# Performance work log

Hardware: AMD Instinct MI355X
Metric: run time of the kernel (lower is better)

## Reference

```python
import jax, jax.numpy as jnp
import numpy as np
import math

B, S, HID = 2, 1024, 2048
H, KV, HD = 32, 8, 64
GROUPS = H // KV
KB_N = 4096
THETA = 10000.0


def _rope_cos_sin(position_ids, head_dim, theta=THETA):
    inv_freq = 1.0 / (theta ** (jnp.arange(0, head_dim, 2, dtype=jnp.float32) / head_dim))
    ang = position_ids.astype(jnp.float32)[..., None] * inv_freq  # [B,S,hd/2]
    cos = jnp.concatenate([jnp.cos(ang), jnp.cos(ang)], -1)[:, None]  # [B,1,S,hd]
    sin = jnp.concatenate([jnp.sin(ang), jnp.sin(ang)], -1)[:, None]
    return cos, sin


def _rotate_half(x):
    h = x.shape[-1] // 2
    return jnp.concatenate([-x[..., h:], x[..., :h]], -1)


def _apply_rope(x, cos, sin):
    return x * cos + _rotate_half(x) * sin


def setup_inputs() -> dict:
    key = jax.random.key(0)
    ks = jax.random.split(key, 10)
    hidden_states = jax.random.normal(ks[0], (B, S, HID), dtype=jnp.float32)
    causal = jnp.where(jnp.tril(jnp.ones((S, S), bool)), 0.0, -1e9).astype(jnp.float32)
    attention_mask = jnp.broadcast_to(causal[None, None], (B, 1, S, S)).copy()
    kb_keys = jax.random.normal(ks[1], (B, KB_N, HD), dtype=jnp.float32)
    kb_values = jax.random.normal(ks[2], (B, KB_N, HD), dtype=jnp.float32)
    position_ids = jnp.broadcast_to(jnp.arange(S, dtype=jnp.int64 if jax.config.read('jax_enable_x64') else jnp.int32)[None], (B, S))
    s = 0.02
    Wq = jax.random.normal(ks[3], (HID, HID), dtype=jnp.float32) * s
    Wq_kb = jax.random.normal(ks[4], (HID, HID), dtype=jnp.float32) * s
    Wk = jax.random.normal(ks[5], (KV * HD, HID), dtype=jnp.float32) * s
    Wv = jax.random.normal(ks[6], (KV * HD, HID), dtype=jnp.float32) * s
    Wo = jax.random.normal(ks[7], (HID, HID), dtype=jnp.float32) * s
    score_shift = jnp.zeros((H, 1), dtype=jnp.float32) - 3.0
    return {"hidden_states": hidden_states, "attention_mask": attention_mask,
            "kb_keys": kb_keys, "kb_values": kb_values, "Wq": Wq, "Wq_kb": Wq_kb,
            "Wk": Wk, "Wv": Wv, "Wo": Wo, "score_shift": score_shift,
            "position_ids": position_ids, "top_k": 128}


def reference(hidden_states, attention_mask, kb_keys, kb_values, Wq, Wq_kb, Wk, Wv, Wo, score_shift, position_ids, top_k):
    bsz, q_len, _ = hidden_states.shape
    scale = 1.0 / math.sqrt(HD)
    q = (hidden_states @ Wq.T).reshape(bsz, q_len, H, HD).transpose(0, 2, 1, 3)
    k = (hidden_states @ Wk.T).reshape(bsz, q_len, KV, HD).transpose(0, 2, 1, 3)
    v = (hidden_states @ Wv.T).reshape(bsz, q_len, KV, HD).transpose(0, 2, 1, 3)
    k = jnp.repeat(k, GROUPS, axis=1)  # repeat_kv
    v = jnp.repeat(v, GROUPS, axis=1)
    cos, sin = _rope_cos_sin(position_ids, HD)
    q = _apply_rope(q, cos, sin)
    k = _apply_rope(k, cos, sin)
    attn = jnp.einsum('bhsd,bhtd->bhst', q, k) * scale
    # KB path (layer_idx=0, kb_layer_frequency=1, sep_query_head, dynamic_sparsify)
    qkb = (hidden_states @ Wq_kb.T).reshape(bsz, q_len, H, HD).transpose(0, 2, 1, 3)
    qkb = _apply_rope(qkb, cos, sin)
    kb_scores = jnp.einsum('bhsd,bnd->bhsn', qkb, kb_keys) * scale  # [B,H,S,N]
    # prune_key_value: top-k over head/seq-summed scores, gather keys/values (no grad)
    top_idx = jax.lax.stop_gradient(jax.lax.top_k(kb_scores.sum((1, 2)), top_k)[1])  # [B,k]
    kb_k_g = jax.lax.stop_gradient(jnp.take_along_axis(kb_keys, top_idx[..., None], axis=1))  # [B,k,hd]
    kb_v_g = jax.lax.stop_gradient(jnp.take_along_axis(kb_values, top_idx[..., None], axis=1))
    kb_w = kb_scores[..., :top_k]  # faithful to original: scores of FIRST top_k columns
    kb_w = kb_w + score_shift.reshape(1, H, 1, 1)
    attn_all = jnp.concatenate([attn, kb_w], -1)
    mask_all = jnp.concatenate([attention_mask, jnp.zeros((bsz, 1, q_len, top_k), attention_mask.dtype)], -1)
    attn_all = attn_all + mask_all
    w = jax.nn.softmax(attn_all.astype(jnp.float32), axis=-1).astype(q.dtype)
    out = jnp.einsum('bhst,bhtd->bhsd', w[..., :q_len], v) \
        + jnp.einsum('bhsk,bkd->bhsd', w[..., q_len:], kb_v_g)
    out = out.transpose(0, 2, 1, 3).reshape(bsz, q_len, HID)
    return out @ Wo.T
```

## Files before the change

kernel.cpp:

```cpp
#include <hip/hip_runtime.h>

constexpr int BB   = 2;
constexpr int SEQ  = 1024;
constexpr int HIDC = 2048;
constexpr int NHEAD = 32;
constexpr int NKVH  = 8;
constexpr int HDIM  = 64;
constexpr int KBN   = 4096;
constexpr int TOPK  = 128;
constexpr int HCH   = 16;

typedef unsigned short ushortt;
typedef __attribute__((ext_vector_type(8))) short short8;
typedef __attribute__((ext_vector_type(4))) float f32x4;

__device__ __forceinline__ ushortt f2b(float f){
  union { float f; unsigned u; } v; v.f = f;
  unsigned r = (v.u + 0x7FFFu + ((v.u >> 16) & 1u)) >> 16;
  return (ushortt)r;
}
__device__ __forceinline__ ushortt f2bfast(float f){
  union { float f; unsigned u; } v; v.f = f;
  return (ushortt)((v.u + 0x8000u) >> 16);
}
__device__ __forceinline__ float b2f(ushortt b){
  union { unsigned u; float f; } v; v.u = ((unsigned)b) << 16;
  return v.f;
}
__device__ __forceinline__ void gload16(const void* g, void* l){
  __builtin_amdgcn_global_load_lds((const __attribute__((address_space(1))) void*)g,
                                   (__attribute__((address_space(3))) void*)l, 16, 0, 0);
}

__global__ __launch_bounds__(256) void cast_all(const float* __restrict__ hs,
    const float* __restrict__ Wq, const float* __restrict__ Wqkb,
    const float* __restrict__ Wk, const float* __restrict__ Wv,
    const float* __restrict__ Wo,
    ushortt* __restrict__ hsb, ushortt* __restrict__ Wcatb, ushortt* __restrict__ Wob)
{
  const size_t NHS = (size_t)BB*SEQ*HIDC;
  const size_t NW  = (size_t)5120*HIDC;
  const size_t NO  = (size_t)HIDC*HIDC;
  const size_t total4 = (NHS + NW + NO) / 4;
  for (size_t i = (size_t)blockIdx.x*256 + threadIdx.x; i < total4; i += (size_t)gridDim.x*256){
    size_t e = i * 4;
    const float* src; ushortt* dst;
    if (e < NHS){ src = hs + e; dst = hsb + e; }
    else if (e < NHS + NW){
      size_t ew = e - NHS; dst = Wcatb + ew;
      if      (ew < (size_t)2048*2048) src = Wq   + ew;
      else if (ew < (size_t)4096*2048) src = Wqkb + (ew - (size_t)2048*2048);
      else if (ew < (size_t)4608*2048) src = Wk   + (ew - (size_t)4096*2048);
      else                             src = Wv   + (ew - (size_t)4608*2048);
    } else { size_t eo = e - NHS - NW; src = Wo + eo; dst = Wob + eo; }
    float4 v = *(const float4*)src;
    dst[0] = f2b(v.x); dst[1] = f2b(v.y); dst[2] = f2b(v.z); dst[3] = f2b(v.w);
  }
}

__global__ void rope_table(const int* __restrict__ pos, float* __restrict__ cosT, float* __restrict__ sinT){
  int idx = blockIdx.x*256 + threadIdx.x;
  if (idx >= BB*SEQ*32) return;
  int i = idx & 31; int bs = idx >> 5;
  int p = pos[bs];
  double invf = exp(-(double)i * (log(10000.0) / 32.0));
  double ang = (double)p * invf;
  cosT[idx] = (float)cos(ang);
  sinT[idx] = (float)sin(ang);
}

template<int OUTF32>
__global__ __launch_bounds__(256) void gemm_bt(const ushortt* __restrict__ A,
                                               const ushortt* __restrict__ Bt,
                                               void* __restrict__ Cv,
                                               int M, int N, int K)
{
  __shared__ ushortt As[2][128*32];
  __shared__ ushortt Bs[2][128*32];
  const int tid = threadIdx.x;
  const int wave = tid >> 6, lane = tid & 63;
  const int bn = blockIdx.x, bm = blockIdx.y;
  const int wr = (wave >> 1) * 64, wc = (wave & 1) * 64;
  const int l4 = lane >> 4, lm = lane & 15;
  f32x4 acc[4][4] = {};
  const int srow = wave*16 + (lane >> 2);
  const int scol = (lane & 3) * 8;
  const ushortt* Ag0 = A  + (size_t)(bm*128 + srow)*K + scol;
  const ushortt* Ag1 = Ag0 + (size_t)64*K;
  const ushortt* Bg0 = Bt + (size_t)(bn*128 + srow)*K + scol;
  const ushortt* Bg1 = Bg0 + (size_t)64*K;
  const int roff = lm*32 + l4*8;
  const int soff = (wave*16)*32;

  auto stage = [&](int k0, ushortt* a, ushortt* b){
    gload16(Ag0 + k0, a + soff);
    gload16(Ag1 + k0, a + 64*32 + soff);
    gload16(Bg0 + k0, b + soff);
    gload16(Bg1 + k0, b + 64*32 + soff);
  };
  auto compute = [&](const ushortt* a, const ushortt* b){
    short8 af[4], bf_[4];
    #pragma unroll
    for (int mi=0;mi<4;++mi) af[mi]  = *(const short8*)&a[(wr + mi*16)*32 + roff];
    #pragma unroll
    for (int ni=0;ni<4;++ni) bf_[ni] = *(const short8*)&b[(wc + ni*16)*32 + roff];
    #pragma unroll
    for (int mi=0;mi<4;++mi)
      #pragma unroll
      for (int ni=0;ni<4;++ni)
        acc[mi][ni] = __builtin_amdgcn_mfma_f32_16x16x32_bf16(af[mi], bf_[ni], acc[mi][ni], 0, 0, 0);
  };

  stage(0, As[0], Bs[0]);
  __syncthreads();
  for (int k0 = 0; k0 < K; k0 += 64){
    stage(k0 + 32, As[1], Bs[1]);
    compute(As[0], Bs[0]);
    __syncthreads();
    if (k0 + 64 < K) stage(k0 + 64, As[0], Bs[0]);
    compute(As[1], Bs[1]);
    __syncthreads();
  }
  const int cr = l4*4;
  #pragma unroll
  for (int mi=0;mi<4;++mi)
    #pragma unroll
    for (int ni=0;ni<4;++ni)
      #pragma unroll
      for (int r=0;r<4;++r){
        size_t row = (size_t)bm*128 + wr + mi*16 + cr + r;
        size_t col = (size_t)bn*128 + wc + ni*16 + lm;
        float v = acc[mi][ni][r];
        if (OUTF32) ((float*)Cv)[row*(size_t)N + col] = v;
        else        ((ushortt*)Cv)[row*(size_t)N + col] = f2b(v);
      }
}

__global__ __launch_bounds__(256) void rope_pack(const ushortt* __restrict__ C1,
    const float* __restrict__ cosT, const float* __restrict__ sinT,
    ushortt* __restrict__ qr, ushortt* __restrict__ qkbr)
{
  const int row = blockIdx.x;
  const int b = row >> 10, s = row & 1023;
  const ushortt* cr = C1 + (size_t)row * 5120;
  const float* ct = cosT + (size_t)row * 32;
  const float* st = sinT + (size_t)row * 32;
  for (int j = threadIdx.x; j < 2048; j += 256){
    int h = j >> 6, d = j & 63, i = d & 31;
    float c = ct[i], sn = st[i];
    int jp = (d < 32) ? j + 32 : j - 32;
    float x  = b2f(cr[j]);
    float xp = b2f(cr[jp]);
    float o = (d < 32) ? (x*c - xp*sn) : (x*c + xp*sn);
    qr[((size_t)(b*NHEAD + h)*SEQ + s)*HDIM + d] = f2b(o * 0.125f);
    float y  = b2f(cr[2048 + j]);
    float yp = b2f(cr[2048 + jp]);
    float o2 = (d < 32) ? (y*c - yp*sn) : (y*c + yp*sn);
    qkbr[((size_t)(b*NHEAD + h)*SEQ + s)*HDIM + d] = f2b(o2 * 0.125f);
  }
}

__global__ __launch_bounds__(256) void kv_pack(const ushortt* __restrict__ C1,
    const float* __restrict__ cosT, const float* __restrict__ sinT,
    ushortt* __restrict__ kr, ushortt* __restrict__ vt)
{
  const int bid = blockIdx.x;
  const int sc  = bid & 15;
  const int kvh = (bid >> 4) & 7;
  const int b   = bid >> 7;
  const int tid = threadIdx.x;
  __shared__ ushortt vs[64][66];
  #pragma unroll
  for (int it = 0; it < 2; ++it){
    int slot = it*256 + tid;
    int s = slot >> 3, dblk = slot & 7;
    const ushortt* base = C1 + (size_t)(b*SEQ + sc*64 + s)*5120 + kvh*64;
    short8 v = *(const short8*)(base + 4608 + dblk*8);
    *(short8*)&vs[s][dblk*8] = v;
    const ushortt* ksrc = base + 4096;
    const float* ct = cosT + ((size_t)b*SEQ + sc*64 + s)*32;
    const float* st = sinT + ((size_t)b*SEQ + sc*64 + s)*32;
    short8 out;
    #pragma unroll
    for (int e=0;e<8;++e){
      int d = dblk*8 + e, i = d & 31;
      int dp = (d < 32) ? d + 32 : d - 32;
      float x = b2f(ksrc[d]), xp = b2f(ksrc[dp]);
      float o = (d < 32) ? (x*ct[i] - xp*st[i]) : (x*ct[i] + xp*st[i]);
      out[e] = (short)f2b(o);
    }
    *(short8*)&kr[((size_t)(b*NKVH + kvh)*SEQ + sc*64 + s)*HDIM + dblk*8] = out;
  }
  __syncthreads();
  #pragma unroll
  for (int it = 0; it < 2; ++it){
    int slot = it*256 + tid;
    int d = slot >> 3, sblk = slot & 7;
    short8 out;
    #pragma unroll
    for (int e=0;e<8;++e) out[e] = (short)vs[sblk*8 + e][d];
    *(short8*)&vt[((size_t)(b*NKVH + kvh)*HDIM + d)*SEQ + sc*64 + sblk*8] = out;
  }
}

__global__ __launch_bounds__(256) void hcs_kernel(const float* __restrict__ hs,
    const float* __restrict__ cosT, const float* __restrict__ sinT,
    float* __restrict__ HcP, float* __restrict__ HsP)
{
  const int b = blockIdx.z, sc = blockIdx.y;
  const int k = blockIdx.x*256 + threadIdx.x;
  const int sbase = sc * (SEQ / HCH);
  __shared__ float cs[64*32];
  __shared__ float sn[64*32];
  for (int t = threadIdx.x; t < 64*32; t += 256){
    cs[t] = cosT[((size_t)b*SEQ + sbase)*32 + t];
    sn[t] = sinT[((size_t)b*SEQ + sbase)*32 + t];
  }
  __syncthreads();
  float ac[32], as_[32];
  #pragma unroll
  for (int i=0;i<32;++i){ ac[i]=0.f; as_[i]=0.f; }
  const float* hp = hs + ((size_t)b*SEQ + sbase)*HIDC + k;
  for (int s = 0; s < 64; ++s){
    float x = hp[(size_t)s*HIDC];
    #pragma unroll
    for (int q=0;q<8;++q){
      float4 c4 = *(const float4*)&cs[s*32 + q*4];
      float4 s4 = *(const float4*)&sn[s*32 + q*4];
      ac[q*4+0]=fmaf(x,c4.x,ac[q*4+0]); as_[q*4+0]=fmaf(x,s4.x,as_[q*4+0]);
      ac[q*4+1]=fmaf(x,c4.y,ac[q*4+1]); as_[q*4+1]=fmaf(x,s4.y,as_[q*4+1]);
      ac[q*4+2]=fmaf(x,c4.z,ac[q*4+2]); as_[q*4+2]=fmaf(x,s4.z,as_[q*4+2]);
      ac[q*4+3]=fmaf(x,c4.w,ac[q*4+3]); as_[q*4+3]=fmaf(x,s4.w,as_[q*4+3]);
    }
  }
  #pragma unroll
  for (int i=0;i<32;++i){
    HcP[(((size_t)sc*BB + b)*32 + i)*HIDC + k] = ac[i];
    HsP[(((size_t)sc*BB + b)*32 + i)*HIDC + k] = as_[i];
  }
}

__global__ __launch_bounds__(256) void hcs_reduce(const float* __restrict__ HcP,
    const float* __restrict__ HsP, float* __restrict__ Hc, float* __restrict__ Hs)
{
  int idx = blockIdx.x*256 + threadIdx.x;
  if (idx >= BB*32*HIDC) return;
  float a = 0.f, c = 0.f;
  #pragma unroll
  for (int sc = 0; sc < HCH; ++sc){
    a += HcP[(size_t)sc*(BB*32*HIDC) + idx];
    c += HsP[(size_t)sc*(BB*32*HIDC) + idx];
  }
  Hc[idx] = a; Hs[idx] = c;
}

__global__ void wsum_kernel(const float* __restrict__ Wqkb, float* __restrict__ Wsum){
  int idx = blockIdx.x*256 + threadIdx.x;
  if (idx >= 64*HIDC) return;
  int d = idx >> 11, k = idx & 2047;
  float acc = 0.f;
  for (int h2 = 0; h2 < NHEAD; ++h2) acc += Wqkb[(size_t)(h2*64 + d)*HIDC + k];
  Wsum[idx] = acc;
}

__global__ __launch_bounds__(256) void qsum_kernel(const float* __restrict__ Hc,
    const float* __restrict__ Hs, const float* __restrict__ Wsum, float* __restrict__ qsum)
{
  const int b = blockIdx.x >> 6, d = blockIdx.x & 63;
  const int i = d & 31;
  const float* hc = Hc + (size_t)(b*32 + i)*HIDC;
  const float* hn = Hs + (size_t)(b*32 + i)*HIDC;
  const float* w1 = Wsum + (size_t)d*HIDC;
  const float* w2 = Wsum + (size_t)((d < 32) ? d + 32 : d - 32)*HIDC;
  double acc = 0.0;
  for (int k = threadIdx.x; k < HIDC; k += 256){
    double t = (double)hc[k] * (double)w1[k];
    double u = (double)hn[k] * (double)w2[k];
    acc += (d < 32) ? (t - u) : (t + u);
  }
  __shared__ double red[256];
  red[threadIdx.x] = acc; __syncthreads();
  for (int s = 128; s > 0; s >>= 1){
    if (threadIdx.x < s) red[threadIdx.x] += red[threadIdx.x + s];
    __syncthreads();
  }
  if (threadIdx.x == 0) qsum[blockIdx.x] = (float)red[0];
}

__global__ void ssum_kernel(const float* __restrict__ qsum, const float* __restrict__ kbK,
                            float* __restrict__ sout){
  int idx = blockIdx.x*256 + threadIdx.x;
  if (idx >= BB*KBN) return;
  int b = idx >> 12;
  const float* q = qsum + b*64;
  const float* kk = kbK + (size_t)idx*64;
  double acc = 0.0;
  for (int d = 0; d < 64; ++d) acc += (double)q[d] * (double)kk[d];
  sout[idx] = (float)(acc * 0.125);
}

__global__ __launch_bounds__(256) void rank_topk(const float* __restrict__ sout,
                                                 int* __restrict__ sel)
{
  const int b = blockIdx.y, chunk = blockIdx.x;
  __shared__ unsigned long long keys[KBN];
  const int tid = threadIdx.x;
  for (int i = tid; i < KBN; i += 256){
    float v = sout[(size_t)b*KBN + i];
    unsigned u = __float_as_uint(v);
    u = (u & 0x80000000u) ? ~u : (u | 0x80000000u);
    keys[i] = ((unsigned long long)u << 32) | (unsigned)(KBN - 1 - i);
  }
  __syncthreads();
  const int myi = chunk*256 + tid;
  const unsigned long long me = keys[myi];
  int rank = 0;
  for (int j = 0; j < KBN; j += 4){
    unsigned long long k0 = keys[j+0];
    unsigned long long k1 = keys[j+1];
    unsigned long long k2 = keys[j+2];
    unsigned long long k3 = keys[j+3];
    rank += (k0 > me) + (k1 > me) + (k2 > me) + (k3 > me);
  }
  if (rank < TOPK) sel[b*TOPK + rank] = myi;
}

__global__ __launch_bounds__(256) void gather_kb(const int* __restrict__ sel,
    const float* __restrict__ kbK, const float* __restrict__ kbV,
    ushortt* __restrict__ kbkb, ushortt* __restrict__ kbvtg)
{
  const int b = blockIdx.x;
  const int tid = threadIdx.x;
  for (int t = tid; t < TOPK*HDIM; t += 256){
    int j = t >> 6, d = t & 63;
    int idx = sel[b*TOPK + j];
    kbkb[(size_t)(b*TOPK + j)*HDIM + d] = f2b(kbK[((size_t)b*KBN + j)*HDIM + d]);
    kbvtg[((size_t)b*HDIM + d)*TOPK + j] = f2b(kbV[((size_t)b*KBN + idx)*HDIM + d]);
  }
}

__global__ __launch_bounds__(256) void attn_kernel(
    const ushortt* __restrict__ qr, const ushortt* __restrict__ qkbr,
    const ushortt* __restrict__ kr, const ushortt* __restrict__ vt,
    const ushortt* __restrict__ kbkb, const ushortt* __restrict__ kbvtg,
    const float* __restrict__ shf, ushortt* __restrict__ attno)
{
  const int i   = blockIdx.x;
  const int xcd = i & 7;
  const int j   = i >> 3;
  const int chunk = xcd + 8*(j >> 5);
  const int pos   = j & 31;
  const int b  = chunk >> 3;
  const int kv = chunk & 7;
  const int qtg = 7 - (pos >> 2);
  const int h  = kv*4 + (pos & 3);
  const int tid = threadIdx.x;
  const int wave = tid >> 6, lane = tid & 63;
  const int l4 = lane >> 4, lm = lane & 15;
  const int qt = qtg*4 + wave;
  const int s0 = qt * 32;

  __shared__ ushortt Ks[2][64*64];
  __shared__ ushortt Vs[2][64*64];
  __shared__ ushortt P[4][32*72];

  ushortt* Pw = P[wave];
  const ushortt* kbase = kr + (size_t)(b*NKVH + kv)*SEQ*HDIM;
  const ushortt* vbase = vt + (size_t)(b*NKVH + kv)*HDIM*SEQ;

  short8 aq[2][2], aqk[2][2];
  {
    const ushortt* qb  = qr   + ((size_t)(b*NHEAD + h)*SEQ + s0)*HDIM;
    const ushortt* qk2 = qkbr + ((size_t)(b*NHEAD + h)*SEQ + s0)*HDIM;
    #pragma unroll
    for (int mi=0;mi<2;++mi)
      #pragma unroll
      for (int kk=0;kk<2;++kk){
        int offa = (mi*16 + lm)*HDIM + kk*32 + l4*8;
        aq[mi][kk]  = *(const short8*)(qb  + offa);
        aqk[mi][kk] = *(const short8*)(qk2 + offa);
      }
  }
  f32x4 O[2][4] = {};
  float lrow[2][4];
  #pragma unroll
  for (int mi=0;mi<2;++mi)
    #pragma unroll
    for (int r=0;r<4;++r) lrow[mi][r] = 0.f;

  auto stageKV = [&](int t, int bsel){
    const int t0 = t*64;
    #pragma unroll
    for (int r2 = 0; r2 < 2; ++r2){
      int slot = r2*256 + wave*64 + lane;
      int row = slot >> 3, cb = slot & 7;
      int lcb = cb ^ (row & 7);
      ushortt* ldsK = &Ks[bsel][(size_t)(r2*256 + wave*64)*8];
      ushortt* ldsV = &Vs[bsel][(size_t)(r2*256 + wave*64)*8];
      gload16(kbase + (size_t)(t0 + row)*HDIM + lcb*8, ldsK);
      gload16(vbase + (size_t)row*SEQ + t0 + lcb*8, ldsV);
    }
  };

  auto update = [&](f32x4 (&lg)[2][4]){
    #pragma unroll
    for (int mi=0;mi<2;++mi)
      #pragma unroll
      for (int r=0;r<4;++r){
        float ps = 0.f;
        #pragma unroll
        for (int ni=0;ni<4;++ni){
          float p = __expf(lg[mi][ni][r]);
          ushortt pb = f2bfast(p);
          ps += b2f(pb);
          Pw[(mi*16 + l4*4 + r)*72 + ni*16 + lm] = pb;
        }
        lrow[mi][r] += ps;
      }
  };

  auto computeTile = [&](int t, int bsel){
    const int t0 = t*64;
    const ushortt* Kb = Ks[bsel];
    const ushortt* Vb = Vs[bsel];
    f32x4 lg[2][4] = {};
    __builtin_amdgcn_s_setprio(1);
    #pragma unroll
    for (int kk=0;kk<2;++kk)
      #pragma unroll
      for (int ni=0;ni<4;++ni){
        int rr = ni*16 + lm;
        int c  = kk*4 + l4;
        short8 bk = *(const short8*)&Kb[rr*64 + ((c ^ (rr&7))*8)];
        lg[0][ni] = __builtin_amdgcn_mfma_f32_16x16x32_bf16(aq[0][kk], bk, lg[0][ni], 0,0,0);
        lg[1][ni] = __builtin_amdgcn_mfma_f32_16x16x32_bf16(aq[1][kk], bk, lg[1][ni], 0,0,0);
      }
    __builtin_amdgcn_s_setprio(0);
    const bool part = (t0 + 63 > s0);
    if (part){
      #pragma unroll
      for (int mi=0;mi<2;++mi)
        #pragma unroll
        for (int ni=0;ni<4;++ni)
          #pragma unroll
          for (int r=0;r<4;++r){
            int row = s0 + mi*16 + l4*4 + r;
            int col = t0 + ni*16 + lm;
            if (col > row) lg[mi][ni][r] = -1e30f;
          }
    }
    update(lg);
    __builtin_amdgcn_s_setprio(1);
    #pragma unroll
    for (int kk=0;kk<2;++kk){
      short8 pa0 = *(const short8*)&Pw[(lm)*72 + kk*32 + l4*8];
      short8 pa1 = *(const short8*)&Pw[(16 + lm)*72 + kk*32 + l4*8];
      #pragma unroll
      for (int di=0;di<4;++di){
        int rr = di*16 + lm;
        int c  = kk*4 + l4;
        short8 bv = *(const short8*)&Vb[rr*64 + ((c ^ (rr&7))*8)];
        O[0][di] = __builtin_amdgcn_mfma_f32_16x16x32_bf16(pa0, bv, O[0][di], 0,0,0);
        O[1][di] = __builtin_amdgcn_mfma_f32_16x16x32_bf16(pa1, bv, O[1][di], 0,0,0);
      }
    }
    __builtin_amdgcn_s_setprio(0);
  };

  const int nkt   = s0/64 + 1;
  const int NTmax = 2*qtg + 2;

  stageKV(0, 0);
  __syncthreads();
  for (int t = 0; t < NTmax; ++t){
    if (t+1 < NTmax) stageKV(t+1, (t+1)&1);
    if (t < nkt) computeTile(t, t&1);
    __syncthreads();
  }

  {
    const float shift = shf[h];
    const ushortt* kbk = kbkb + (size_t)b*TOPK*HDIM;
    const ushortt* kbv = kbvtg + (size_t)b*HDIM*TOPK;
    #pragma unroll
    for (int jt=0;jt<2;++jt){
      const int j0 = jt*64;
      f32x4 lg[2][4] = {};
      __builtin_amdgcn_s_setprio(1);
      #pragma unroll
      for (int kk=0;kk<2;++kk)
        #pragma unroll
        for (int ni=0;ni<4;++ni){
          short8 bk = *(const short8*)(kbk + (size_t)(j0 + ni*16 + lm)*HDIM + kk*32 + l4*8);
          lg[0][ni] = __builtin_amdgcn_mfma_f32_16x16x32_bf16(aqk[0][kk], bk, lg[0][ni], 0,0,0);
          lg[1][ni] = __builtin_amdgcn_mfma_f32_16x16x32_bf16(aqk[1][kk], bk, lg[1][ni], 0,0,0);
        }
      __builtin_amdgcn_s_setprio(0);
      #pragma unroll
      for (int mi=0;mi<2;++mi)
        #pragma unroll
        for (int ni=0;ni<4;++ni)
          #pragma unroll
          for (int r=0;r<4;++r)
            lg[mi][ni][r] += shift;
      update(lg);
      __builtin_amdgcn_s_setprio(1);
      #pragma unroll
      for (int kk=0;kk<2;++kk){
        short8 pa0 = *(const short8*)&Pw[(lm)*72 + kk*32 + l4*8];
        short8 pa1 = *(const short8*)&Pw[(16 + lm)*72 + kk*32 + l4*8];
        #pragma unroll
        for (int di=0;di<4;++di){
          short8 bv = *(const short8*)(kbv + (size_t)(di*16 + lm)*TOPK + j0 + kk*32 + l4*8);
          O[0][di] = __builtin_amdgcn_mfma_f32_16x16x32_bf16(pa0, bv, O[0][di], 0,0,0);
          O[1][di] = __builtin_amdgcn_mfma_f32_16x16x32_bf16(pa1, bv, O[1][di], 0,0,0);
        }
      }
      __builtin_amdgcn_s_setprio(0);
    }
  }
  #pragma unroll
  for (int mi=0;mi<2;++mi)
    #pragma unroll
    for (int r=0;r<4;++r){
      float ls = lrow[mi][r];
      ls += __shfl_xor(ls, 1);
      ls += __shfl_xor(ls, 2);
      ls += __shfl_xor(ls, 4);
      ls += __shfl_xor(ls, 8);
      lrow[mi][r] = 1.0f / ls;
    }
  #pragma unroll
  for (int mi=0;mi<2;++mi)
    #pragma unroll
    for (int di=0;di<4;++di)
      #pragma unroll
      for (int r=0;r<4;++r){
        float o = O[mi][di][r] * lrow[mi][r];
        attno[(size_t)(b*SEQ + s0 + mi*16 + l4*4 + r)*HIDC + h*HDIM + di*16 + lm] = f2b(o);
      }
}

extern "C" void kernel_launch(void* const* d_in, const int* in_sizes, int n_in,
                              void* d_out, int out_size, void* d_ws, size_t ws_size,
                              hipStream_t stream)
{
  (void)in_sizes; (void)n_in; (void)out_size; (void)ws_size;
  const float* hs   = (const float*)d_in[0];
  const float* kbK  = (const float*)d_in[2];
  const float* kbV  = (const float*)d_in[3];
  const float* Wq   = (const float*)d_in[4];
  const float* Wqkb = (const float*)d_in[5];
  const float* Wk   = (const float*)d_in[6];
  const float* Wv   = (const float*)d_in[7];
  const float* Wo   = (const float*)d_in[8];
  const float* shf  = (const float*)d_in[9];
  const int*   pos  = (const int*)d_in[10];

  char* w = (char*)d_ws;
  size_t off = 0;
  auto alloc = [&](size_t bytes)->void*{
    void* p = w + off; off += (bytes + 255) & ~(size_t)255; return p;
  };
  ushortt* hsb   = (ushortt*)alloc((size_t)2048*2048*2);
  ushortt* Wcatb = (ushortt*)alloc((size_t)5120*2048*2);
  ushortt* Wob   = (ushortt*)alloc((size_t)2048*2048*2);
  ushortt* C1    = (ushortt*)alloc((size_t)2048*5120*2);
  float*   cosT  = (float*)alloc((size_t)BB*SEQ*32*4);
  float*   sinT  = (float*)alloc((size_t)BB*SEQ*32*4);
  ushortt* qr    = (ushortt*)alloc((size_t)BB*NHEAD*SEQ*HDIM*2);
  ushortt* qkbr  = (ushortt*)alloc((size_t)BB*NHEAD*SEQ*HDIM*2);
  ushortt* kr    = (ushortt*)alloc((size_t)BB*NKVH*SEQ*HDIM*2);
  ushortt* vt    = (ushortt*)alloc((size_t)BB*NKVH*SEQ*HDIM*2);
  float*   Hc    = (float*)alloc((size_t)BB*32*HIDC*4);
  float*   Hs    = (float*)alloc((size_t)BB*32*HIDC*4);
  float*   Wsum  = (float*)alloc((size_t)64*HIDC*4);
  float*   qsum  = (float*)alloc((size_t)BB*64*4);
  float*   sbuf  = (float*)alloc((size_t)BB*KBN*4);
  int*     sel   = (int*)alloc((size_t)BB*TOPK*4);
  ushortt* kbkb  = (ushortt*)alloc((size_t)BB*TOPK*HDIM*2);
  ushortt* kbvtg = (ushortt*)alloc((size_t)BB*HDIM*TOPK*2);
  ushortt* attno = (ushortt*)alloc((size_t)2048*2048*2);

  float* HcP = (float*)C1;
  float* HsP = HcP + (size_t)HCH*BB*32*HIDC;

  rope_table<<<dim3(256), dim3(256), 0, stream>>>(pos, cosT, sinT);
  hcs_kernel<<<dim3(8, HCH, BB), dim3(256), 0, stream>>>(hs, cosT, sinT, HcP, HsP);
  hcs_reduce<<<dim3(512), dim3(256), 0, stream>>>(HcP, HsP, Hc, Hs);
  wsum_kernel<<<dim3(512), dim3(256), 0, stream>>>(Wqkb, Wsum);
  qsum_kernel<<<dim3(128), dim3(256), 0, stream>>>(Hc, Hs, Wsum, qsum);
  ssum_kernel<<<dim3(32), dim3(256), 0, stream>>>(qsum, kbK, sbuf);
  rank_topk<<<dim3(KBN/256, BB), dim3(256), 0, stream>>>(sbuf, sel);
  gather_kb<<<dim3(BB), dim3(256), 0, stream>>>(sel, kbK, kbV, kbkb, kbvtg);
  cast_all<<<dim3(2048), dim3(256), 0, stream>>>(hs, Wq, Wqkb, Wk, Wv, Wo, hsb, Wcatb, Wob);
  gemm_bt<0><<<dim3(40, 16), dim3(256), 0, stream>>>(hsb, Wcatb, (void*)C1, 2048, 5120, 2048);
  rope_pack<<<dim3(2048), dim3(256), 0, stream>>>(C1, cosT, sinT, qr, qkbr);
  kv_pack<<<dim3(256), dim3(256), 0, stream>>>(C1, cosT, sinT, kr, vt);
  attn_kernel<<<dim3(512), dim3(256), 0, stream>>>(qr, qkbr, kr, vt, kbkb, kbvtg, shf, attno);
  gemm_bt<1><<<dim3(16, 16), dim3(256), 0, stream>>>(attno, Wob, d_out, 2048, 2048, 2048);
}
```

Measured before the change: 309.4 us.

## Prefetch two stages ahead with partial vmcnt waits in GEMM and attention loops

Both the GEMM main loop and the attention KV loop now issue two async global-to-LDS stages up front. Each iteration waits only for the older stage using s_waitcnt vmcnt(4) plus raw s_barrier, rather than a full __syncthreads drain. This keeps one load in flight while computing, so memory latency overlaps with MFMA work. The risk is correctness if the vmcnt count does not match the number of loads each stage issues. The sched_barriers also limit how the compiler can interleave instructions.

Result: faster. 300.7 us (-2.8%).

```diff
diff --git a/kernel.cpp b/kernel.cpp
--- a/kernel.cpp
+++ b/kernel.cpp
@@ -92,13 +92,15 @@
   const int roff = lm*32 + l4*8;
   const int soff = (wave*16)*32;
 
-  auto stage = [&](int k0, ushortt* a, ushortt* b){
-    gload16(Ag0 + k0, a + soff);
-    gload16(Ag1 + k0, a + 64*32 + soff);
-    gload16(Bg0 + k0, b + soff);
-    gload16(Bg1 + k0, b + 64*32 + soff);
+  auto stage = [&](int k0, int bsel){
+    gload16(Ag0 + k0, As[bsel] + soff);
+    gload16(Ag1 + k0, As[bsel] + 64*32 + soff);
+    gload16(Bg0 + k0, Bs[bsel] + soff);
+    gload16(Bg1 + k0, Bs[bsel] + 64*32 + soff);
   };
-  auto compute = [&](const ushortt* a, const ushortt* b){
+  auto compute = [&](int bsel){
+    const ushortt* a = As[bsel];
+    const ushortt* b = Bs[bsel];
     short8 af[4], bf_[4];
     #pragma unroll
     for (int mi=0;mi<4;++mi) af[mi]  = *(const short8*)&a[(wr + mi*16)*32 + roff];
@@ -111,16 +113,23 @@
         acc[mi][ni] = __builtin_amdgcn_mfma_f32_16x16x32_bf16(af[mi], bf_[ni], acc[mi][ni], 0, 0, 0);
   };
 
-  stage(0, As[0], Bs[0]);
-  __syncthreads();
-  for (int k0 = 0; k0 < K; k0 += 64){
-    stage(k0 + 32, As[1], Bs[1]);
-    compute(As[0], Bs[0]);
-    __syncthreads();
-    if (k0 + 64 < K) stage(k0 + 64, As[0], Bs[0]);
-    compute(As[1], Bs[1]);
-    __syncthreads();
-  }
+  stage(0, 0);
+  if (32 < K) stage(32, 1);
+  int bsel = 0;
+  for (int k0 = 0; k0 < K; k0 += 32){
+    if (k0 + 32 < K) { asm volatile("s_waitcnt vmcnt(4)" ::: "memory"); }
+    else             { asm volatile("s_waitcnt vmcnt(0)" ::: "memory"); }
+    __builtin_amdgcn_sched_barrier(0);
+    __builtin_amdgcn_s_barrier();
+    __builtin_amdgcn_sched_barrier(0);
+    compute(bsel);
+    __builtin_amdgcn_sched_barrier(0);
+    __builtin_amdgcn_s_barrier();
+    __builtin_amdgcn_sched_barrier(0);
+    if (k0 + 64 < K) stage(k0 + 64, bsel);
+    bsel ^= 1;
+  }
+
   const int cr = l4*4;
   #pragma unroll
   for (int mi=0;mi<4;++mi)
@@ -471,11 +480,18 @@
   const int NTmax = 2*qtg + 2;
 
   stageKV(0, 0);
-  __syncthreads();
+  if (NTmax > 1) stageKV(1, 1);
   for (int t = 0; t < NTmax; ++t){
-    if (t+1 < NTmax) stageKV(t+1, (t+1)&1);
+    if (t < NTmax - 1) { asm volatile("s_waitcnt vmcnt(4)" ::: "memory"); }
+    else               { asm volatile("s_waitcnt vmcnt(0)" ::: "memory"); }
+    __builtin_amdgcn_sched_barrier(0);
+    __builtin_amdgcn_s_barrier();
+    __builtin_amdgcn_sched_barrier(0);
     if (t < nkt) computeTile(t, t&1);
-    __syncthreads();
+    __builtin_amdgcn_sched_barrier(0);
+    __builtin_amdgcn_s_barrier();
+    __builtin_amdgcn_sched_barrier(0);
+    if (t+2 < NTmax) stageKV(t+2, t&1);
   }
 
   {
```
